# Optimization experiments

Hardware: AMD Instinct MI355X
Metric: run time of the kernel (lower is better)

The kernel has to match this reference:

```python
import jax, jax.numpy as jnp
import numpy as np

L = 500_000      # total nodes across all graphs
D = 256          # d_model
G = 4096         # number of graphs
EPS_SOFTMAX = 1e-7
EPS_LN = 1e-5


def setup_inputs() -> dict:
    key = jax.random.key(0)
    ks = jax.random.split(key, 6)
    f_node = jax.random.normal(ks[0], (L, D), dtype=jnp.float32)
    key_W = jax.random.normal(ks[1], (D, D), dtype=jnp.float32) * 0.02
    key_b = jnp.zeros((D,), dtype=jnp.float32)
    value_W = jax.random.normal(ks[2], (D, D), dtype=jnp.float32) * 0.02
    value_b = jnp.zeros((D,), dtype=jnp.float32)
    gamma = jnp.ones((D,), dtype=jnp.float32)
    beta = jnp.zeros((D,), dtype=jnp.float32)
    graph_id = jax.random.randint(ks[3], (L,), 0, G, dtype=jnp.int32)
    return {
        "f_node": f_node,
        "key_W": key_W,
        "key_b": key_b,
        "value_W": value_W,
        "value_b": value_b,
        "gamma": gamma,
        "beta": beta,
        "graph_id": graph_id,
        "num_graphs": G,
    }


def reference(f_node, key_W, key_b, value_W, value_b, gamma, beta, graph_id, num_graphs):
    # attn scores: Linear(key)  -> [L, D]
    attn = f_node @ key_W.T + key_b
    # scatter_softmax over nodes within each graph (per feature column)
    seg_max = jax.ops.segment_max(attn, graph_id, num_segments=num_graphs)  # [G, D]
    ex = jnp.exp(attn - seg_max[graph_id])                                   # [L, D]
    seg_sum = jax.ops.segment_sum(ex, graph_id, num_segments=num_graphs)    # [G, D]
    attn = ex / (seg_sum[graph_id] + EPS_SOFTMAX)
    # weighted aggregation of value projection -> [G, D]
    val = f_node @ value_W.T + value_b
    f_graph = jax.ops.segment_sum(val * attn, graph_id, num_segments=num_graphs)
    # LayerNorm (dropout is identity in eval mode)
    mu = jnp.mean(f_graph, axis=-1, keepdims=True)
    var = jnp.mean(jnp.square(f_graph - mu), axis=-1, keepdims=True)
    return (f_graph - mu) * jax.lax.rsqrt(var + EPS_LN) * gamma + beta
```

## Files before the change

### kernel.cpp

```cpp
#include <hip/hip_runtime.h>

typedef short short8 __attribute__((ext_vector_type(8)));
typedef float floatx4 __attribute__((ext_vector_type(4)));

#define GPB 16
#define ORD_CAP 2304

__device__ __forceinline__ unsigned short f2bf(float x) {
  union { float f; unsigned int u; } c; c.f = x;
  return (unsigned short)((c.u + 0x7FFFu + ((c.u >> 16) & 1u)) >> 16);
}

__device__ __forceinline__ unsigned cvtpk(float lo, float hi) {
  unsigned r;
  asm("v_cvt_pk_bf16_f32 %0, %1, %2" : "=v"(r) : "v"(lo), "v"(hi));
  return r;
}

__device__ __forceinline__ void gld16(const void* g, void* l) {
  __builtin_amdgcn_global_load_lds((const __attribute__((address_space(1))) void*)g,
                                   (__attribute__((address_space(3))) void*)l, 16, 0, 0);
}

__global__ void k_hist(const int* __restrict__ gid, int L, int* __restrict__ counts) {
  int i = blockIdx.x * blockDim.x + threadIdx.x;
  if (i < L) atomicAdd(&counts[gid[i]], 1);
}

__global__ void k_scan(const int* __restrict__ counts, int* __restrict__ offsets,
                       int* __restrict__ cursor, int G) {
  __shared__ int sc[1024];
  int t = threadIdx.x;
  int items = (G + 1023) >> 10;
  int base = t * items;
  int s = 0;
  for (int i = 0; i < items; ++i) { int idx = base + i; if (idx < G) s += counts[idx]; }
  sc[t] = s;
  __syncthreads();
  for (int off = 1; off < 1024; off <<= 1) {
    int v = (t >= off) ? sc[t - off] : 0;
    __syncthreads();
    if (t >= off) sc[t] += v;
    __syncthreads();
  }
  int run = (t == 0) ? 0 : sc[t - 1];
  for (int i = 0; i < items; ++i) {
    int idx = base + i;
    if (idx < G) { offsets[idx] = run; cursor[idx] = run; run += counts[idx]; }
  }
  if (t == 1023) offsets[G] = sc[1023];
}

__global__ void k_scatter(const int* __restrict__ gid, int L, int* __restrict__ cursor,
                          int* __restrict__ order) {
  int i = blockIdx.x * blockDim.x + threadIdx.x;
  if (i < L) {
    int g = gid[i];
    int pos = atomicAdd(&cursor[g], 1);
    order[pos] = i;
  }
}

__global__ void k_prepw(const float* __restrict__ keyW, const float* __restrict__ valW,
                        unsigned short* __restrict__ W2) {
  int j2 = blockIdx.x;
  int k = threadIdx.x;
  int wv = j2 >> 6, half = (j2 >> 5) & 1, c = j2 & 31;
  int d = (wv << 5) + c;
  const float* src = half ? valW : keyW;
  W2[j2 * 256 + k] = f2bf(src[d * 256 + k]);
}

__launch_bounds__(512, 1)
__global__ void k_fused(const float* __restrict__ fnode,
                        const unsigned short* __restrict__ W2,
                        const float* __restrict__ key_b, const float* __restrict__ value_b,
                        const float* __restrict__ gamma, const float* __restrict__ beta,
                        const int* __restrict__ order, const int* __restrict__ offsets,
                        float* __restrict__ out, int L, int Gtot) {
  __shared__ __align__(16) float As[2][64 * 256];
  __shared__ int ord_s[ORD_CAP];
  __shared__ float fg[GPB][256];
  __shared__ int eb[GPB + 1];
  __shared__ float redS[4], redS2[4];

  const int t = threadIdx.x;
  const int lane = t & 63;
  const int w = t >> 6;
  const int lcol = lane & 15;
  const int lrow = lane >> 4;
  const int g0 = blockIdx.x * GPB;

  if (t <= GPB) eb[t] = offsets[min(g0 + t, Gtot)];
  __syncthreads();
  const int rbase = eb[0];
  const int span = eb[GPB] - rbase;
  const int nc = max(1, (span + 63) >> 6);

  for (int i = t; i < ORD_CAP; i += 512) ord_s[i] = order[min(rbase + i, L - 1)];

  float kb[2], vb[2];
#pragma unroll
  for (int nj = 0; nj < 2; ++nj) {
    int d = (w << 5) + (nj << 4) + lcol;
    kb[nj] = key_b[d];
    vb[nj] = value_b[d];
  }
  const unsigned short* Wn[4];
#pragma unroll
  for (int nj = 0; nj < 4; ++nj)
    Wn[nj] = W2 + ((size_t)((w << 6) + ((nj >> 1) << 5) + ((nj & 1) << 4) + lcol)) * 256 +
             lrow * 8;
  short8 bp[4][4];
#pragma unroll
  for (int nj = 0; nj < 4; ++nj)
#pragma unroll
    for (int kk = 0; kk < 4; ++kk)
      bp[nj][kk] = *reinterpret_cast<const short8*>(Wn[nj] + (kk << 5));

  __syncthreads();

  auto stage = [&](int c, int buf) {
    const int m0 = c << 6;
#pragma unroll
    for (int it = 0; it < 8; ++it) {
      int gi = m0 + (w << 3) + it;
      if (gi > span - 1) gi = span - 1;
      const int idx = (gi < ORD_CAP) ? ord_s[gi] : order[rbase + gi];
      const char* gsrc =
          (const char*)fnode + ((size_t)idx << 10) + ((lane << 4) ^ (it << 4));
      gld16(gsrc, (char*)&As[buf][0] + (((w << 3) + it) << 10));
    }
  };

  stage(0, 0);
  if (nc > 1) {
    stage(1, 1);
    asm volatile("s_waitcnt vmcnt(8)" ::: "memory");
  } else {
    asm volatile("s_waitcnt vmcnt(0)" ::: "memory");
  }
  __builtin_amdgcn_s_barrier();

  int curg = 0, flushed = 0;
  int ecur = eb[1] - rbase;
  float den[2] = {0.f, 0.f};
  float num[2] = {0.f, 0.f};

  for (int c = 0; c < nc; ++c) {
    const char* AsB = (const char*)&As[c & 1][0];
    floatx4 acc[4][4];
#pragma unroll
    for (int mi = 0; mi < 4; ++mi)
#pragma unroll
      for (int nj = 0; nj < 4; ++nj)
        acc[mi][nj] = (floatx4){0.f, 0.f, 0.f, 0.f};

    __builtin_amdgcn_s_setprio(1);
#pragma unroll
    for (int kk = 0; kk < 8; ++kk) {
      short8 afr[4];
#pragma unroll
      for (int mi = 0; mi < 4; ++mi) {
        const int row = mi * 16 + lcol;
        const int x7 = row & 7;
        const int s0 = (kk * 8 + lrow * 2) ^ x7;
        const int s1 = (kk * 8 + lrow * 2 + 1) ^ x7;
        const floatx4 lo = *reinterpret_cast<const floatx4*>(AsB + (row << 10) + (s0 << 4));
        const floatx4 hi = *reinterpret_cast<const floatx4*>(AsB + (row << 10) + (s1 << 4));
        union { unsigned u[4]; short8 s; } cc;
        cc.u[0] = cvtpk(lo[0], lo[1]);
        cc.u[1] = cvtpk(lo[2], lo[3]);
        cc.u[2] = cvtpk(hi[0], hi[1]);
        cc.u[3] = cvtpk(hi[2], hi[3]);
        afr[mi] = cc.s;
      }
#pragma unroll
      for (int nj = 0; nj < 4; ++nj) {
        const short8 bfr = (kk < 4)
                               ? bp[nj][kk]
                               : *reinterpret_cast<const short8*>(Wn[nj] + (kk << 5));
#pragma unroll
        for (int mi = 0; mi < 4; ++mi)
          acc[mi][nj] =
              __builtin_amdgcn_mfma_f32_16x16x32_bf16(afr[mi], bfr, acc[mi][nj], 0, 0, 0);
      }
    }
    __builtin_amdgcn_s_setprio(0);

    const int m0 = c << 6;
    {
      int lo = 0;
      while (true) {
        const int hi = min(ecur - m0, 64);
#pragma unroll
        for (int mi = 0; mi < 4; ++mi)
#pragma unroll
          for (int qq = 0; qq < 4; ++qq) {
            const int r = mi * 16 + lrow * 4 + qq;
            const bool in = (r >= lo) && (r < hi);
#pragma unroll
            for (int nj = 0; nj < 2; ++nj) {
              const float a = acc[mi][nj][qq] + kb[nj];
              const float v = acc[mi][nj + 2][qq] + vb[nj];
              const float e_ = in ? __expf(a) : 0.f;
              den[nj] += e_;
              num[nj] += v * e_;
            }
          }
        if (ecur <= m0 + 64) {
#pragma unroll
          for (int nj = 0; nj < 2; ++nj) {
            float ds = den[nj], ns = num[nj];
            ds += __shfl_xor(ds, 16, 64);
            ds += __shfl_xor(ds, 32, 64);
            ns += __shfl_xor(ns, 16, 64);
            ns += __shfl_xor(ns, 32, 64);
            if (lrow == 0)
              fg[curg & (GPB - 1)][(w << 5) + (nj << 4) + lcol] = ns / (ds + 1e-7f);
            den[nj] = 0.f;
            num[nj] = 0.f;
          }
          ++curg;
          lo = hi;
          ecur = (curg < GPB) ? (eb[curg + 1] - rbase) : 0x7fffffff;
        } else
          break;
        if (curg >= GPB) break;
      }
    }

    if (curg > flushed) {
      asm volatile("s_waitcnt lgkmcnt(0)" ::: "memory");
      __builtin_amdgcn_s_barrier();
      for (int j = flushed; j < curg; ++j) {
        float x = 0.f;
        if (t < 256) x = fg[j & (GPB - 1)][t];
        float s = x, s2 = x * x;
#pragma unroll
        for (int o = 32; o > 0; o >>= 1) {
          s += __shfl_xor(s, o, 64);
          s2 += __shfl_xor(s2, o, 64);
        }
        if (t < 256 && lane == 0) { redS[w] = s; redS2[w] = s2; }
        asm volatile("s_waitcnt lgkmcnt(0)" ::: "memory");
        __builtin_amdgcn_s_barrier();
        if (t < 256 && (g0 + j) < Gtot) {
          const float ts = redS[0] + redS[1] + redS[2] + redS[3];
          const float ts2 = redS2[0] + redS2[1] + redS2[2] + redS2[3];
          const float mu = ts * (1.f / 256.f);
          const float var = ts2 * (1.f / 256.f) - mu * mu;
          const float inv = rsqrtf(var + 1e-5f);
          out[(size_t)(g0 + j) * 256 + t] = (x - mu) * inv * gamma[t] + beta[t];
        }
        __builtin_amdgcn_s_barrier();
      }
      flushed = curg;
    }

    __builtin_amdgcn_s_barrier();
    if (c + 2 < nc) stage(c + 2, c & 1);
    if (c + 1 < nc) {
      if (c + 2 < nc)
        asm volatile("s_waitcnt vmcnt(8)" ::: "memory");
      else
        asm volatile("s_waitcnt vmcnt(0)" ::: "memory");
      __builtin_amdgcn_s_barrier();
    }
  }
}

extern "C" void kernel_launch(void* const* d_in, const int* in_sizes, int n_in,
                              void* d_out, int out_size, void* d_ws, size_t ws_size,
                              hipStream_t stream) {
  const float* f_node   = (const float*)d_in[0];
  const float* key_W    = (const float*)d_in[1];
  const float* key_b    = (const float*)d_in[2];
  const float* value_W  = (const float*)d_in[3];
  const float* value_b  = (const float*)d_in[4];
  const float* gamma    = (const float*)d_in[5];
  const float* beta     = (const float*)d_in[6];
  const int*   graph_id = (const int*)d_in[7];
  const int L = in_sizes[0] / 256;
  const int G = out_size / 256;

  char* ws = (char*)d_ws;
  size_t off = 0;
  int* order = (int*)(ws + off); off += (size_t)L * 4;
  off = (off + 255) & ~(size_t)255;
  int* counts = (int*)(ws + off); off += (size_t)G * 4;
  int* offsets = (int*)(ws + off); off += (size_t)(G + 1) * 4;
  int* cursor = (int*)(ws + off); off += (size_t)G * 4;
  off = (off + 255) & ~(size_t)255;
  unsigned short* W2 = (unsigned short*)(ws + off); off += 512 * 256 * 2;

  hipMemsetAsync(counts, 0, (size_t)G * 4, stream);
  k_hist<<<(L + 255) / 256, 256, 0, stream>>>(graph_id, L, counts);
  k_scan<<<1, 1024, 0, stream>>>(counts, offsets, cursor, G);
  k_scatter<<<(L + 255) / 256, 256, 0, stream>>>(graph_id, L, cursor, order);
  k_prepw<<<512, 256, 0, stream>>>(key_W, value_W, W2);
  const int nblk = (G + GPB - 1) / GPB;
  k_fused<<<nblk, 512, 0, stream>>>(f_node, W2, key_b, value_b, gamma, beta, order,
                                    offsets, (float*)d_out, L, G);
}
```

Baseline: 424.7 us.

## Software-pipeline MFMA and softmax epilogue across chunks, defer LayerNorm to end

Restructures the main loop so the MFMA work for chunk c runs alongside the exp/accumulate epilogue for chunk c-1, using two accumulator register sets (accA/accB). This lets the epilogue's ALU and transcendental work interleave with matrix instructions instead of running serially after them. It also adds a fast path that skips per-row range checks when a chunk lies entirely inside one graph. The per-chunk LayerNorm flush with its barriers is replaced by a single pass over all GPB graphs at the end. Holding two 4x4 floatx4 accumulator sets raises register pressure and may lower occupancy or cause spills. The s_setprio hints are removed.

Result: slower. 867.3 us (+104.2%).

```diff
diff --git a/kernel.cpp b/kernel.cpp
--- a/kernel.cpp
+++ b/kernel.cpp
@@ -133,30 +133,13 @@
     }
   };
 
-  stage(0, 0);
-  if (nc > 1) {
-    stage(1, 1);
-    asm volatile("s_waitcnt vmcnt(8)" ::: "memory");
-  } else {
-    asm volatile("s_waitcnt vmcnt(0)" ::: "memory");
-  }
-  __builtin_amdgcn_s_barrier();
-
-  int curg = 0, flushed = 0;
-  int ecur = eb[1] - rbase;
-  float den[2] = {0.f, 0.f};
-  float num[2] = {0.f, 0.f};
-
-  for (int c = 0; c < nc; ++c) {
+  auto mfma_chunk = [&](floatx4 (&acc)[4][4], int c) {
     const char* AsB = (const char*)&As[c & 1][0];
-    floatx4 acc[4][4];
 #pragma unroll
     for (int mi = 0; mi < 4; ++mi)
 #pragma unroll
       for (int nj = 0; nj < 4; ++nj)
         acc[mi][nj] = (floatx4){0.f, 0.f, 0.f, 0.f};
-
-    __builtin_amdgcn_s_setprio(1);
 #pragma unroll
     for (int kk = 0; kk < 8; ++kk) {
       short8 afr[4];
@@ -186,87 +169,117 @@
               __builtin_amdgcn_mfma_f32_16x16x32_bf16(afr[mi], bfr, acc[mi][nj], 0, 0, 0);
       }
     }
-    __builtin_amdgcn_s_setprio(0);
-
+  };
+
+  int curg = 0;
+  int ecur = eb[1] - rbase;
+  float den[2] = {0.f, 0.f};
+  float num[2] = {0.f, 0.f};
+
+  auto epi_chunk = [&](floatx4 (&acc)[4][4], int c) {
     const int m0 = c << 6;
-    {
-      int lo = 0;
-      while (true) {
-        const int hi = min(ecur - m0, 64);
-#pragma unroll
-        for (int mi = 0; mi < 4; ++mi)
-#pragma unroll
-          for (int qq = 0; qq < 4; ++qq) {
-            const int r = mi * 16 + lrow * 4 + qq;
-            const bool in = (r >= lo) && (r < hi);
-#pragma unroll
-            for (int nj = 0; nj < 2; ++nj) {
-              const float a = acc[mi][nj][qq] + kb[nj];
-              const float v = acc[mi][nj + 2][qq] + vb[nj];
-              const float e_ = in ? __expf(a) : 0.f;
-              den[nj] += e_;
-              num[nj] += v * e_;
-            }
+    int lo = 0;
+    while (true) {
+      const int hi = min(ecur - m0, 64);
+      const bool full = (lo == 0) && (hi >= 64);
+#pragma unroll
+      for (int mi = 0; mi < 4; ++mi)
+#pragma unroll
+        for (int qq = 0; qq < 4; ++qq) {
+          const int r = mi * 16 + lrow * 4 + qq;
+          const bool in = full || ((r >= lo) && (r < hi));
+#pragma unroll
+          for (int nj = 0; nj < 2; ++nj) {
+            const float a = acc[mi][nj][qq] + kb[nj];
+            const float v = acc[mi][nj + 2][qq] + vb[nj];
+            const float e_ = in ? __expf(a) : 0.f;
+            den[nj] += e_;
+            num[nj] += v * e_;
           }
-        if (ecur <= m0 + 64) {
-#pragma unroll
-          for (int nj = 0; nj < 2; ++nj) {
-            float ds = den[nj], ns = num[nj];
-            ds += __shfl_xor(ds, 16, 64);
-            ds += __shfl_xor(ds, 32, 64);
-            ns += __shfl_xor(ns, 16, 64);
-            ns += __shfl_xor(ns, 32, 64);
-            if (lrow == 0)
-              fg[curg & (GPB - 1)][(w << 5) + (nj << 4) + lcol] = ns / (ds + 1e-7f);
-            den[nj] = 0.f;
-            num[nj] = 0.f;
-          }
-          ++curg;
-          lo = hi;
-          ecur = (curg < GPB) ? (eb[curg + 1] - rbase) : 0x7fffffff;
-        } else
-          break;
-        if (curg >= GPB) break;
-      }
-    }
-
-    if (curg > flushed) {
-      asm volatile("s_waitcnt lgkmcnt(0)" ::: "memory");
-      __builtin_amdgcn_s_barrier();
-      for (int j = flushed; j < curg; ++j) {
-        float x = 0.f;
-        if (t < 256) x = fg[j & (GPB - 1)][t];
-        float s = x, s2 = x * x;
-#pragma unroll
-        for (int o = 32; o > 0; o >>= 1) {
-          s += __shfl_xor(s, o, 64);
-          s2 += __shfl_xor(s2, o, 64);
         }
-        if (t < 256 && lane == 0) { redS[w] = s; redS2[w] = s2; }
-        asm volatile("s_waitcnt lgkmcnt(0)" ::: "memory");
-        __builtin_amdgcn_s_barrier();
-        if (t < 256 && (g0 + j) < Gtot) {
-          const float ts = redS[0] + redS[1] + redS[2] + redS[3];
-          const float ts2 = redS2[0] + redS2[1] + redS2[2] + redS2[3];
-          const float mu = ts * (1.f / 256.f);
-          const float var = ts2 * (1.f / 256.f) - mu * mu;
-          const float inv = rsqrtf(var + 1e-5f);
-          out[(size_t)(g0 + j) * 256 + t] = (x - mu) * inv * gamma[t] + beta[t];
+      if (ecur <= m0 + 64) {
+#pragma unroll
+        for (int nj = 0; nj < 2; ++nj) {
+          float ds = den[nj], ns = num[nj];
+          ds += __shfl_xor(ds, 16, 64);
+          ds += __shfl_xor(ds, 32, 64);
+          ns += __shfl_xor(ns, 16, 64);
+          ns += __shfl_xor(ns, 32, 64);
+          if (lrow == 0)
+            fg[curg & (GPB - 1)][(w << 5) + (nj << 4) + lcol] = ns / (ds + 1e-7f);
+          den[nj] = 0.f;
+          num[nj] = 0.f;
         }
-        __builtin_amdgcn_s_barrier();
-      }
-      flushed = curg;
+        ++curg;
+        lo = hi;
+        ecur = (curg < GPB) ? (eb[curg + 1] - rbase) : 0x7fffffff;
+      } else
+        break;
+      if (curg >= GPB) break;
+    }
+  };
+
+  floatx4 accA[4][4], accB[4][4];
+
+  stage(0, 0);
+  if (nc > 1) {
+    stage(1, 1);
+    asm volatile("s_waitcnt vmcnt(8)" ::: "memory");
+  } else {
+    asm volatile("s_waitcnt vmcnt(0)" ::: "memory");
+  }
+  __builtin_amdgcn_s_barrier();
+
+  mfma_chunk(accA, 0);
+  __builtin_amdgcn_s_barrier();
+  if (2 < nc) stage(2, 0);
+
+  for (int c = 1; c < nc; ++c) {
+    if (c + 1 < nc)
+      asm volatile("s_waitcnt vmcnt(8)" ::: "memory");
+    else
+      asm volatile("s_waitcnt vmcnt(0)" ::: "memory");
+    __builtin_amdgcn_s_barrier();
+
+    if (c & 1) {
+      mfma_chunk(accB, c);
+      epi_chunk(accA, c - 1);
+    } else {
+      mfma_chunk(accA, c);
+      epi_chunk(accB, c - 1);
     }
 
     __builtin_amdgcn_s_barrier();
     if (c + 2 < nc) stage(c + 2, c & 1);
-    if (c + 1 < nc) {
-      if (c + 2 < nc)
-        asm volatile("s_waitcnt vmcnt(8)" ::: "memory");
-      else
-        asm volatile("s_waitcnt vmcnt(0)" ::: "memory");
-      __builtin_amdgcn_s_barrier();
-    }
+  }
+
+  if ((nc - 1) & 1)
+    epi_chunk(accB, nc - 1);
+  else
+    epi_chunk(accA, nc - 1);
+
+  __syncthreads();
+
+  for (int j = 0; j < GPB; ++j) {
+    float x = 0.f;
+    if (t < 256) x = fg[j][t];
+    float s = x, s2 = x * x;
+#pragma unroll
+    for (int o = 32; o > 0; o >>= 1) {
+      s += __shfl_xor(s, o, 64);
+      s2 += __shfl_xor(s2, o, 64);
+    }
+    if (t < 256 && lane == 0) { redS[w] = s; redS2[w] = s2; }
+    __syncthreads();
+    if (t < 256 && (g0 + j) < Gtot) {
+      const float ts = redS[0] + redS[1] + redS[2] + redS[3];
+      const float ts2 = redS2[0] + redS2[1] + redS2[2] + redS2[3];
+      const float mu = ts * (1.f / 256.f);
+      const float var = ts2 * (1.f / 256.f) - mu * mu;
+      const float inv = rsqrtf(var + 1e-5f);
+      out[(size_t)(g0 + j) * 256 + t] = (x - mu) * inv * gamma[t] + beta[t];
+    }
+    __syncthreads();
   }
 }
 
```
